# Optimization experiments

Measured on AMD Instinct MI355X. Metric: run time of the kernel, lower is better.

## Reference

```python
import jax, jax.numpy as jnp
import numpy as np

# Module constants (match init_kwargs / input_specs)
B, Q, K, DM, H, F, S = 2, 2048, 2048, 512, 8, 5, 2
DH = DM // H  # head dim = 64


def setup_inputs() -> dict:
    key = jax.random.key(0)
    ks_ = jax.random.split(key, 18)
    sc = 1.0 / np.sqrt(DM)
    inp = {
        'qs': jax.random.normal(ks_[0], (B, Q, DM), jnp.float32),
        'ks': jax.random.normal(ks_[1], (B, K, DM), jnp.float32),
        'vs': jax.random.normal(ks_[2], (B, K, DM), jnp.float32),
        'qs_locs': jax.random.uniform(ks_[3], (B, Q, S), jnp.float32) * 10.0,
        'ks_locs': jax.random.uniform(ks_[4], (B, K, S), jnp.float32) * 10.0,
        # projection weights (MLP([512]) == single Dense(512))
        'Wq': jax.random.normal(ks_[5], (DM, DM), jnp.float32) * sc,
        'bq': jnp.zeros((DM,), jnp.float32),
        'Wk': jax.random.normal(ks_[6], (DM, DM), jnp.float32) * sc,
        'bk': jnp.zeros((DM,), jnp.float32),
        'Wv': jax.random.normal(ks_[7], (DM, DM), jnp.float32) * sc,
        'bv': jnp.zeros((DM,), jnp.float32),
        'Wo': jax.random.normal(ks_[8], (DM, DM), jnp.float32) * sc,
        'bo': jnp.zeros((DM,), jnp.float32),
        # TISA RBF params, one triple per (head, basis); init near module defaults (1,1,0)
        'a': 1.0 + 0.1 * jax.random.normal(ks_[9], (H * F,), jnp.float32),
        'b': 1.0 + 0.1 * jax.random.normal(ks_[10], (H * F,), jnp.float32),
        'c': 0.1 * jax.random.normal(ks_[11], (H * F,), jnp.float32),
        # valid lens in [K//2, K] so every row has at least one valid key
        'valid_lens': jax.random.randint(ks_[12], (B,), K // 2, K + 1).astype(jnp.int32),
    }
    return inp


def reference(qs, ks, vs, qs_locs, ks_locs, Wq, bq, Wk, bk, Wv, bv, Wo, bo, a, b, c, valid_lens):
    # Projections and head split
    q = (qs @ Wq + bq).reshape(B, Q, H, DH) / jnp.sqrt(jnp.float32(DH))
    k = (ks @ Wk + bk).reshape(B, K, H, DH)
    v = (vs @ Wv + bv).reshape(B, K, H, DH)

    # Pairwise L2 distance between query and key locations: [B, Q, K]
    diff = qs_locs[:, :, None, :] - ks_locs[:, None, :, :]
    d = jnp.sqrt(jnp.sum(diff * diff, axis=-1))

    # TISA RBF bias, summed over F basis functions per head: [B, H, Q, K]
    aH, bH, cH = a.reshape(H, F), b.reshape(H, F), c.reshape(H, F)
    bias = jnp.zeros((B, H, Q, K), jnp.float32)
    for f in range(F):  # small fixed loop over basis functions
        af = aH[:, f][None, :, None, None]
        bf = jnp.abs(bH[:, f])[None, :, None, None]
        cf = cH[:, f][None, :, None, None]
        bias = bias + af * jnp.exp(-bf * (d[:, None] - cf) ** 2)

    scores = jnp.einsum('bqhd,bkhd->bhqk', q, k) + bias
    mask = (jnp.arange(K)[None, :] < valid_lens[:, None])[:, None, None, :]  # [B,1,1,K]
    scores = jnp.where(mask, scores, -jnp.inf)
    p = jax.nn.softmax(scores, axis=-1)  # identical to the online-softmax scan result
    ctx = jnp.einsum('bhqk,bkhd->bqhd', p, v).reshape(B, Q, DM)
    return ctx @ Wo + bo
```

## Files before the change

### kernel.cpp

```cpp
#include <hip/hip_runtime.h>
#include <hip/hip_fp16.h>

typedef unsigned short u16;
typedef __bf16 bf16x8 __attribute__((ext_vector_type(8)));
typedef float f32x4 __attribute__((ext_vector_type(4)));
typedef float f32x16 __attribute__((ext_vector_type(16)));

#define MFMA16(a, b, c) __builtin_amdgcn_mfma_f32_16x16x32_bf16(a, b, c, 0, 0, 0)
#define MFMA32(a, b, c) __builtin_amdgcn_mfma_f32_32x32x16_bf16(a, b, c, 0, 0, 0)

constexpr float LOG2E = 1.44269504088896340736f;

__device__ __forceinline__ u16 f2bf(float x) {
  unsigned u = __float_as_uint(x);
  u += 0x7fffu + ((u >> 16) & 1u);
  return (u16)(u >> 16);
}
__device__ __forceinline__ u16 f2bf_fast(float x) {
  return (u16)((__float_as_uint(x) + 0x8000u) >> 16);
}

struct FalseT { static constexpr bool value = false; };
struct TrueT  { static constexpr bool value = true;  };

__global__ void transpose_w_kernel(const float* __restrict__ w0, const float* __restrict__ w1,
                                   const float* __restrict__ w2, const float* __restrict__ w3,
                                   u16* __restrict__ wt) {
  __shared__ float tile[32][33];
  const float* W = blockIdx.z == 0 ? w0 : blockIdx.z == 1 ? w1 : blockIdx.z == 2 ? w2 : w3;
  u16* T = wt + (size_t)blockIdx.z * 512 * 512;
  int tx = threadIdx.x, ty = threadIdx.y;
  int x = blockIdx.x * 32 + tx;
  int y0 = blockIdx.y * 32;
#pragma unroll
  for (int i = 0; i < 32; i += 8) tile[ty + i][tx] = W[(y0 + ty + i) * 512 + x];
  __syncthreads();
  int xo = blockIdx.y * 32 + tx;
  int r0 = blockIdx.x * 32;
#pragma unroll
  for (int i = 0; i < 32; i += 8) T[(r0 + ty + i) * 512 + xo] = f2bf(tile[tx][ty + i]);
}

__global__ __launch_bounds__(256) void qkv_gemm(
    const float* __restrict__ qs, const float* __restrict__ ks, const float* __restrict__ vs,
    const u16* __restrict__ Wt, const float* __restrict__ bq, const float* __restrict__ bk,
    const float* __restrict__ bv, u16* __restrict__ qg, u16* __restrict__ kg,
    u16* __restrict__ vTg) {
  __shared__ u16 As[128 * 72];
  __shared__ u16 Bs[64 * 72];
  const int tid = threadIdx.x;
  const int wave = tid >> 6, lane = tid & 63;
  const int l15 = lane & 15, quad = lane >> 4;
  const int id = blockIdx.x;
  const bool qk = id < 512;
  int z = 0, m0, n0;
  const float* Af = nullptr;
  const u16* Ab = nullptr;
  const u16* Bb = nullptr;
  const float* Bf = nullptr;
  if (qk) {
    z = id >> 8;
    int t = id & 255;
    m0 = (t >> 3) * 128;
    n0 = (t & 7) * 64;
    Af = z ? ks : qs;
    Bb = Wt + z * 262144;
  } else {
    int t = id - 512;
    m0 = (t >> 6) * 128;
    n0 = (t & 63) * 64;
    Ab = Wt + 2 * 262144;
    Bf = vs;
  }
  f32x4 acc[2][4];
#pragma unroll
  for (int i = 0; i < 2; i++)
#pragma unroll
    for (int j = 0; j < 4; j++) {
      f32x4 zr = {0.f, 0.f, 0.f, 0.f};
      acc[i][j] = zr;
    }
  const int srA = tid >> 1, scA = (tid & 1) * 32;
  const int srB = tid >> 2, scB = (tid & 3) * 16;
  for (int k0 = 0; k0 < 512; k0 += 64) {
    if (qk) {
      const float* ga = Af + (m0 + srA) * 512 + k0 + scA;
      u16* la = As + srA * 72 + scA;
#pragma unroll
      for (int c = 0; c < 4; ++c) {
        float4 f0 = *(const float4*)(ga + c * 8);
        float4 f1 = *(const float4*)(ga + c * 8 + 4);
        uint4 u;
        u.x = f2bf(f0.x) | ((unsigned)f2bf(f0.y) << 16);
        u.y = f2bf(f0.z) | ((unsigned)f2bf(f0.w) << 16);
        u.z = f2bf(f1.x) | ((unsigned)f2bf(f1.y) << 16);
        u.w = f2bf(f1.z) | ((unsigned)f2bf(f1.w) << 16);
        *(uint4*)(la + c * 8) = u;
      }
      const u16* gb = Bb + (n0 + srB) * 512 + k0 + scB;
      u16* lb = Bs + srB * 72 + scB;
      *(uint4*)(lb) = *(const uint4*)(gb);
      *(uint4*)(lb + 8) = *(const uint4*)(gb + 8);
    } else {
      const u16* ga = Ab + (m0 + srA) * 512 + k0 + scA;
      u16* la = As + srA * 72 + scA;
#pragma unroll
      for (int c = 0; c < 4; ++c) *(uint4*)(la + c * 8) = *(const uint4*)(ga + c * 8);
      const float* gb = Bf + (n0 + srB) * 512 + k0 + scB;
      u16* lb = Bs + srB * 72 + scB;
#pragma unroll
      for (int c = 0; c < 2; ++c) {
        float4 f0 = *(const float4*)(gb + c * 8);
        float4 f1 = *(const float4*)(gb + c * 8 + 4);
        uint4 u;
        u.x = f2bf(f0.x) | ((unsigned)f2bf(f0.y) << 16);
        u.y = f2bf(f0.z) | ((unsigned)f2bf(f0.w) << 16);
        u.z = f2bf(f1.x) | ((unsigned)f2bf(f1.y) << 16);
        u.w = f2bf(f1.z) | ((unsigned)f2bf(f1.w) << 16);
        *(uint4*)(lb + c * 8) = u;
      }
    }
    __syncthreads();
#pragma unroll
    for (int st = 0; st < 2; ++st) {
      bf16x8 af[2], bfr[4];
#pragma unroll
      for (int mt = 0; mt < 2; ++mt)
        af[mt] = *(const bf16x8*)(As + (wave * 32 + mt * 16 + l15) * 72 + st * 32 + quad * 8);
#pragma unroll
      for (int nt = 0; nt < 4; ++nt)
        bfr[nt] = *(const bf16x8*)(Bs + (nt * 16 + l15) * 72 + st * 32 + quad * 8);
#pragma unroll
      for (int mt = 0; mt < 2; ++mt)
#pragma unroll
        for (int nt = 0; nt < 4; ++nt) acc[mt][nt] = MFMA16(af[mt], bfr[nt], acc[mt][nt]);
    }
    __syncthreads();
  }
  if (qk) {
    const float* bias = z ? bk : bq;
    const float scale = z ? 1.0f : 0.125f * LOG2E;
    u16* outp = z ? kg : qg;
#pragma unroll
    for (int mt = 0; mt < 2; ++mt)
#pragma unroll
      for (int nt = 0; nt < 4; ++nt)
#pragma unroll
        for (int r = 0; r < 4; ++r) {
          int row = m0 + wave * 32 + mt * 16 + quad * 4 + r;
          int col = n0 + nt * 16 + l15;
          float v = (acc[mt][nt][r] + bias[col]) * scale;
          int b = row >> 11, q = row & 2047, h = col >> 6, dh = col & 63;
          outp[(((b * 8 + h) * 2048) + q) * 64 + dh] = f2bf(v);
        }
  } else {
#pragma unroll
    for (int mt = 0; mt < 2; ++mt)
#pragma unroll
      for (int nt = 0; nt < 4; ++nt)
#pragma unroll
        for (int r = 0; r < 4; ++r) {
          int row = m0 + wave * 32 + mt * 16 + quad * 4 + r;
          int col = n0 + nt * 16 + l15;
          vTg[row * 4096 + col] = f2bf(acc[mt][nt][r] + bv[row]);
        }
  }
}

__global__ __launch_bounds__(256, 4) void attn_kernel(
    const u16* __restrict__ qg, const u16* __restrict__ kg, const u16* __restrict__ vTg,
    const float* __restrict__ qlocs, const float* __restrict__ klocs,
    const float* __restrict__ aP, const float* __restrict__ bP, const float* __restrict__ cP,
    const int* __restrict__ vlen, u16* __restrict__ Opart, float* __restrict__ lpart) {
  constexpr int TBLN = 1024;
  constexpr float DMAX = 14.16f;
  constexpr float TSCALE = (float)TBLN / DMAX;
  __shared__ u16 Ks[64 * 72];
  __shared__ u16 Vs[64 * 72];
  __shared__ u16 Ps[4][32 * 68];
  __shared__ alignas(16) float2 kloc_s[64];
  __shared__ unsigned tbl[TBLN];
  const int tid = threadIdx.x;
  const int wave = tid >> 6, lane = tid & 63;
  const int l31 = lane & 31, hi = lane >> 5;
  const int bh = blockIdx.y, b = bh >> 3, h = bh & 7;
  const int z = blockIdx.z;
  const int vl = vlen[b];
  const int ntiles = (vl + 63) >> 6;
  const int nfull = vl >> 6;
  const int tb = ntiles >> 2, rem = ntiles & 3;
  const int kt0 = z * tb + (z < rem ? z : rem);
  const int ktend = kt0 + tb + (z < rem ? 1 : 0);

  for (int i = tid; i < TBLN; i += 256) {
    float d0 = i * (DMAX / TBLN), d1 = (i + 1) * (DMAX / TBLN);
    float g0 = 0.f, g1 = 0.f;
#pragma unroll
    for (int f = 0; f < 5; ++f) {
      float af = aP[h * 5 + f], bf = fabsf(bP[h * 5 + f]), cf = cP[h * 5 + f];
      float t0 = d0 - cf, t1 = d1 - cf;
      g0 += af * __expf(-bf * t0 * t0);
      g1 += af * __expf(-bf * t1 * t1);
    }
    g0 *= LOG2E;
    g1 *= LOG2E;
    unsigned lo = __half_as_ushort(__float2half(g0));
    unsigned hi_ = __half_as_ushort(__float2half(g1 - g0));
    tbl[i] = lo | (hi_ << 16);
  }

  const int qrow = blockIdx.x * 128 + wave * 32 + l31;
  bf16x8 aq[4];
  {
    const u16* qr = qg + (bh * 2048 + qrow) * 64 + hi * 8;
#pragma unroll
    for (int st = 0; st < 4; ++st) aq[st] = *(const bf16x8*)(qr + st * 16);
  }
  float qpx, qpy;
  {
    float2 p = *(const float2*)(qlocs + (b * 2048 + qrow) * 2);
    qpx = p.x * TSCALE;
    qpy = p.y * TSCALE;
  }
  float l_ = 0.f;
  f32x16 oacc[2];
#pragma unroll
  for (int i = 0; i < 2; ++i)
#pragma unroll
    for (int j = 0; j < 16; ++j) oacc[i][j] = 0.f;

  const int srow = tid >> 2, scol = (tid & 3) * 16;
  const u16* gk_base = kg + (bh * 2048 + srow) * 64 + scol;
  const u16* gv_base = vTg + (h * 64 + srow) * 4096 + b * 2048 + scol;
  const float* kl_base = klocs + (b * 2048 + tid) * 2;
  u16* pw = Ps[wave];

  auto tile = [&](int kt, auto mc) {
    constexpr bool MASKED = decltype(mc)::value;
    const int k0 = kt * 64;
    {
      const u16* gk = gk_base + k0 * 64;
      u16* lk = Ks + srow * 72 + scol;
      *(uint4*)(lk) = *(const uint4*)(gk);
      *(uint4*)(lk + 8) = *(const uint4*)(gk + 8);
      const u16* gv = gv_base + k0;
      u16* lv = Vs + srow * 72 + scol;
      *(uint4*)(lv) = *(const uint4*)(gv);
      *(uint4*)(lv + 8) = *(const uint4*)(gv + 8);
      if (tid < 64) {
        float2 kl = *(const float2*)(kl_base + k0 * 2);
        kloc_s[tid] = make_float2(kl.x * TSCALE, kl.y * TSCALE);
      }
    }
    __syncthreads();
    f32x16 s[2];
#pragma unroll
    for (int t = 0; t < 2; ++t) {
#pragma unroll
      for (int j = 0; j < 16; ++j) s[t][j] = 0.f;
#pragma unroll
      for (int st = 0; st < 4; ++st) {
        bf16x8 kf = *(const bf16x8*)(Ks + (t * 32 + l31) * 72 + st * 16 + hi * 8);
        s[t] = MFMA32(kf, aq[st], s[t]);
      }
    }
#pragma unroll
    for (int t = 0; t < 2; ++t)
#pragma unroll
      for (int g = 0; g < 4; ++g) {
        const int kl0 = t * 32 + hi * 4 + g * 8;
        float4 ka = *(const float4*)(&kloc_s[kl0]);
        float4 kb = *(const float4*)(&kloc_s[kl0 + 2]);
        float kx[4] = {ka.x, ka.z, kb.x, kb.z};
        float ky[4] = {ka.y, ka.w, kb.y, kb.w};
        float p[4];
#pragma unroll
        for (int j = 0; j < 4; ++j) {
          float dx = qpx - kx[j], dy = qpy - ky[j];
          float t_ = __builtin_amdgcn_sqrtf(fmaf(dx, dx, dy * dy));
          int ti = (int)t_;
          float fr = t_ - (float)ti;
          unsigned e = tbl[ti];
          float gg = __half2float(__ushort_as_half((u16)(e & 0xffffu)));
          float dg = __half2float(__ushort_as_half((u16)(e >> 16)));
          float v = s[t][g * 4 + j] + fmaf(fr, dg, gg);
          if (MASKED) v = (k0 + kl0 + j < vl) ? v : -1e30f;
          p[j] = __builtin_amdgcn_exp2f(v);
          l_ += p[j];
        }
        uint2 w;
        w.x = f2bf_fast(p[0]) | ((unsigned)f2bf_fast(p[1]) << 16);
        w.y = f2bf_fast(p[2]) | ((unsigned)f2bf_fast(p[3]) << 16);
        *(uint2*)(pw + l31 * 68 + kl0) = w;
      }
    __asm__ volatile("s_waitcnt lgkmcnt(0)" ::: "memory");
#pragma unroll
    for (int st = 0; st < 4; ++st) {
      bf16x8 pf = *(const bf16x8*)(pw + l31 * 68 + st * 16 + hi * 8);
#pragma unroll
      for (int h2 = 0; h2 < 2; ++h2) {
        bf16x8 vf = *(const bf16x8*)(Vs + (h2 * 32 + l31) * 72 + st * 16 + hi * 8);
        oacc[h2] = MFMA32(vf, pf, oacc[h2]);
      }
    }
    __syncthreads();
  };

  const int fullend = ktend < nfull ? ktend : nfull;
  for (int kt = kt0; kt < fullend; ++kt) tile(kt, FalseT{});
  if (ktend > nfull) tile(nfull, TrueT{});

  l_ += __shfl_xor(l_, 32);
  if (hi == 0) lpart[z * 32768 + bh * 2048 + qrow] = l_;
  u16* ob = Opart + ((size_t)(z * 16 + bh) * 2048 + qrow) * 64;
#pragma unroll
  for (int h2 = 0; h2 < 2; ++h2)
#pragma unroll
    for (int g = 0; g < 4; ++g) {
      const int dh0 = h2 * 32 + hi * 4 + g * 8;
      uint2 w;
      w.x = f2bf(oacc[h2][g * 4 + 0]) | ((unsigned)f2bf(oacc[h2][g * 4 + 1]) << 16);
      w.y = f2bf(oacc[h2][g * 4 + 2]) | ((unsigned)f2bf(oacc[h2][g * 4 + 3]) << 16);
      *(uint2*)(ob + dh0) = w;
    }
}

__global__ __launch_bounds__(256) void out_gemm(
    const u16* __restrict__ Opart, const float* __restrict__ lpart,
    const u16* __restrict__ Wt, const float* __restrict__ bo, float* __restrict__ out) {
  __shared__ u16 As[128 * 72];
  __shared__ u16 Bs[64 * 72];
  const u16* WoT = Wt + 3 * 262144;
  const int tid = threadIdx.x;
  const int wave = tid >> 6, lane = tid & 63;
  const int l15 = lane & 15, quad = lane >> 4;
  const int m0 = blockIdx.x * 128, n0 = blockIdx.y * 64;
  f32x4 acc[2][4];
#pragma unroll
  for (int i = 0; i < 2; i++)
#pragma unroll
    for (int j = 0; j < 4; j++) {
      f32x4 zr = {0.f, 0.f, 0.f, 0.f};
      acc[i][j] = zr;
    }
  const int srA = tid >> 1, scA = (tid & 1) * 32;
  const int srB = tid >> 2, scB = (tid & 3) * 16;
  const int row = m0 + srA, b = row >> 11, qq = row & 2047;
  for (int k0 = 0; k0 < 512; k0 += 64) {
    const int h = k0 >> 6;
    const int base = (b * 8 + h) * 2048 + qq;
    float l = lpart[base] + lpart[32768 + base] + lpart[2 * 32768 + base] +
              lpart[3 * 32768 + base];
    const float inv = 1.f / l;
    float vals[32];
#pragma unroll
    for (int e = 0; e < 32; ++e) vals[e] = 0.f;
#pragma unroll
    for (int zz = 0; zz < 4; ++zz) {
      const u16* op = Opart + ((size_t)(zz * 32768) + base) * 64 + scA;
#pragma unroll
      for (int c = 0; c < 4; ++c) {
        bf16x8 o8 = *(const bf16x8*)(op + c * 8);
#pragma unroll
        for (int j = 0; j < 8; ++j) vals[c * 8 + j] += (float)o8[j];
      }
    }
    u16* la = As + srA * 72 + scA;
#pragma unroll
    for (int c = 0; c < 4; ++c) {
      uint4 u;
      u.x = f2bf(vals[c * 8 + 0] * inv) | ((unsigned)f2bf(vals[c * 8 + 1] * inv) << 16);
      u.y = f2bf(vals[c * 8 + 2] * inv) | ((unsigned)f2bf(vals[c * 8 + 3] * inv) << 16);
      u.z = f2bf(vals[c * 8 + 4] * inv) | ((unsigned)f2bf(vals[c * 8 + 5] * inv) << 16);
      u.w = f2bf(vals[c * 8 + 6] * inv) | ((unsigned)f2bf(vals[c * 8 + 7] * inv) << 16);
      *(uint4*)(la + c * 8) = u;
    }
    const u16* gb = WoT + (n0 + srB) * 512 + k0 + scB;
    u16* lb = Bs + srB * 72 + scB;
    *(uint4*)(lb) = *(const uint4*)(gb);
    *(uint4*)(lb + 8) = *(const uint4*)(gb + 8);
    __syncthreads();
#pragma unroll
    for (int st = 0; st < 2; ++st) {
      bf16x8 af[2], bfr[4];
#pragma unroll
      for (int mt = 0; mt < 2; ++mt)
        af[mt] = *(const bf16x8*)(As + (wave * 32 + mt * 16 + l15) * 72 + st * 32 + quad * 8);
#pragma unroll
      for (int nt = 0; nt < 4; ++nt)
        bfr[nt] = *(const bf16x8*)(Bs + (nt * 16 + l15) * 72 + st * 32 + quad * 8);
#pragma unroll
      for (int mt = 0; mt < 2; ++mt)
#pragma unroll
        for (int nt = 0; nt < 4; ++nt) acc[mt][nt] = MFMA16(af[mt], bfr[nt], acc[mt][nt]);
    }
    __syncthreads();
  }
#pragma unroll
  for (int mt = 0; mt < 2; ++mt)
#pragma unroll
    for (int nt = 0; nt < 4; ++nt)
#pragma unroll
      for (int r = 0; r < 4; ++r) {
        int rrow = m0 + wave * 32 + mt * 16 + quad * 4 + r;
        int col = n0 + nt * 16 + l15;
        out[rrow * 512 + col] = acc[mt][nt][r] + bo[col];
      }
}

extern "C" void kernel_launch(void* const* d_in, const int* in_sizes, int n_in, void* d_out,
                              int out_size, void* d_ws, size_t ws_size, hipStream_t stream) {
  const float* qs = (const float*)d_in[0];
  const float* ks = (const float*)d_in[1];
  const float* vs = (const float*)d_in[2];
  const float* qlocs = (const float*)d_in[3];
  const float* klocs = (const float*)d_in[4];
  const float* Wq = (const float*)d_in[5];
  const float* bq = (const float*)d_in[6];
  const float* Wk = (const float*)d_in[7];
  const float* bk = (const float*)d_in[8];
  const float* Wv = (const float*)d_in[9];
  const float* bv = (const float*)d_in[10];
  const float* Wo = (const float*)d_in[11];
  const float* bo = (const float*)d_in[12];
  const float* aP = (const float*)d_in[13];
  const float* bP = (const float*)d_in[14];
  const float* cP = (const float*)d_in[15];
  const int* vlen = (const int*)d_in[16];
  float* out = (float*)d_out;

  u16* Wt = (u16*)d_ws;
  u16* qg = Wt + 4 * 262144;
  u16* kg = qg + 2097152;
  u16* vTg = kg + 2097152;
  u16* Opart = vTg + 2097152;
  float* lpart = (float*)(Opart + (size_t)4 * 2097152);

  transpose_w_kernel<<<dim3(16, 16, 4), dim3(32, 8), 0, stream>>>(Wq, Wk, Wv, Wo, Wt);
  qkv_gemm<<<768, 256, 0, stream>>>(qs, ks, vs, Wt, bq, bk, bv, qg, kg, vTg);
  attn_kernel<<<dim3(16, 16, 4), 256, 0, stream>>>(qg, kg, vTg, qlocs, klocs, aP, bP, cP, vlen,
                                                   Opart, lpart);
  out_gemm<<<dim3(32, 8), 256, 0, stream>>>(Opart, lpart, Wt, bo, out);
}
```

Before: 198.0 us.

## Pre-swizzle K/V into MFMA fragment layout and load directly from global

The projection kernel now writes K and V in a per-tile fragment-ordered layout matching the MFMA operand register layout. The attention kernel then loads K/V fragments straight from global memory into registers, dropping the shared-memory staging of K and V and the two block-wide barriers per tile. Key locations for the block's whole key range are preloaded once into a larger shared buffer. In exchange, every wave in the block re-reads the same K/V from global/L2 (4x redundant traffic), and load latency is no longer hidden behind LDS staging.

```diff
diff --git a/kernel.cpp b/kernel.cpp
--- a/kernel.cpp
+++ b/kernel.cpp
@@ -140,7 +140,6 @@
   if (qk) {
     const float* bias = z ? bk : bq;
     const float scale = z ? 1.0f : 0.125f * LOG2E;
-    u16* outp = z ? kg : qg;
 #pragma unroll
     for (int mt = 0; mt < 2; ++mt)
 #pragma unroll
@@ -150,8 +149,16 @@
           int row = m0 + wave * 32 + mt * 16 + quad * 4 + r;
           int col = n0 + nt * 16 + l15;
           float v = (acc[mt][nt][r] + bias[col]) * scale;
-          int b = row >> 11, q = row & 2047, h = col >> 6, dh = col & 63;
-          outp[(((b * 8 + h) * 2048) + q) * 64 + dh] = f2bf(v);
+          int b = row >> 11, key = row & 2047, hh = col >> 6, dh = col & 63;
+          int bhh = b * 8 + hh;
+          if (z == 0) {
+            qg[((bhh * 2048) + key) * 64 + dh] = f2bf(v);
+          } else {
+            int kt = key >> 6, tt = (key >> 5) & 1, lk = key & 31;
+            int st = dh >> 4, hif = (dh >> 3) & 1, j = dh & 7;
+            kg[(size_t)(bhh * 32 + kt) * 4096 + tt * 2048 + st * 512 + (hif * 32 + lk) * 8 +
+               j] = f2bf(v);
+          }
         }
   } else {
 #pragma unroll
@@ -162,23 +169,26 @@
         for (int r = 0; r < 4; ++r) {
           int row = m0 + wave * 32 + mt * 16 + quad * 4 + r;
           int col = n0 + nt * 16 + l15;
-          vTg[row * 4096 + col] = f2bf(acc[mt][nt][r] + bv[row]);
+          int hh = row >> 6, dh = row & 63, b = col >> 11, key = col & 2047;
+          int bhh = b * 8 + hh;
+          int kt = key >> 6, kk = key & 63, st = kk >> 4, hif = (kk >> 3) & 1, j = kk & 7;
+          int h2 = dh >> 5, lk = dh & 31;
+          vTg[(size_t)(bhh * 32 + kt) * 4096 + h2 * 2048 + st * 512 + (hif * 32 + lk) * 8 + j] =
+              f2bf(acc[mt][nt][r] + bv[row]);
         }
   }
 }
 
 __global__ __launch_bounds__(256, 4) void attn_kernel(
-    const u16* __restrict__ qg, const u16* __restrict__ kg, const u16* __restrict__ vTg,
+    const u16* __restrict__ qg, const u16* __restrict__ kfrag, const u16* __restrict__ vfrag,
     const float* __restrict__ qlocs, const float* __restrict__ klocs,
     const float* __restrict__ aP, const float* __restrict__ bP, const float* __restrict__ cP,
     const int* __restrict__ vlen, u16* __restrict__ Opart, float* __restrict__ lpart) {
   constexpr int TBLN = 1024;
   constexpr float DMAX = 14.16f;
   constexpr float TSCALE = (float)TBLN / DMAX;
-  __shared__ u16 Ks[64 * 72];
-  __shared__ u16 Vs[64 * 72];
   __shared__ u16 Ps[4][32 * 68];
-  __shared__ alignas(16) float2 kloc_s[64];
+  __shared__ alignas(16) float2 klb[640];
   __shared__ unsigned tbl[TBLN];
   const int tid = threadIdx.x;
   const int wave = tid >> 6, lane = tid & 63;
@@ -208,6 +218,12 @@
     unsigned hi_ = __half_as_ushort(__float2half(g1 - g0));
     tbl[i] = lo | (hi_ << 16);
   }
+  const int nk = (ktend - kt0) * 64;
+  for (int i = tid; i < nk; i += 256) {
+    float2 kl = *(const float2*)(klocs + (b * 2048 + kt0 * 64 + i) * 2);
+    klb[i] = make_float2(kl.x * TSCALE, kl.y * TSCALE);
+  }
+  __syncthreads();
 
   const int qrow = blockIdx.x * 128 + wave * 32 + l31;
   bf16x8 aq[4];
@@ -228,49 +244,30 @@
   for (int i = 0; i < 2; ++i)
 #pragma unroll
     for (int j = 0; j < 16; ++j) oacc[i][j] = 0.f;
-
-  const int srow = tid >> 2, scol = (tid & 3) * 16;
-  const u16* gk_base = kg + (bh * 2048 + srow) * 64 + scol;
-  const u16* gv_base = vTg + (h * 64 + srow) * 4096 + b * 2048 + scol;
-  const float* kl_base = klocs + (b * 2048 + tid) * 2;
   u16* pw = Ps[wave];
 
   auto tile = [&](int kt, auto mc) {
     constexpr bool MASKED = decltype(mc)::value;
     const int k0 = kt * 64;
-    {
-      const u16* gk = gk_base + k0 * 64;
-      u16* lk = Ks + srow * 72 + scol;
-      *(uint4*)(lk) = *(const uint4*)(gk);
-      *(uint4*)(lk + 8) = *(const uint4*)(gk + 8);
-      const u16* gv = gv_base + k0;
-      u16* lv = Vs + srow * 72 + scol;
-      *(uint4*)(lv) = *(const uint4*)(gv);
-      *(uint4*)(lv + 8) = *(const uint4*)(gv + 8);
-      if (tid < 64) {
-        float2 kl = *(const float2*)(kl_base + k0 * 2);
-        kloc_s[tid] = make_float2(kl.x * TSCALE, kl.y * TSCALE);
-      }
-    }
-    __syncthreads();
-    f32x16 s[2];
+    const int rt64 = (kt - kt0) * 64;
+    const u16* fb = kfrag + (size_t)(bh * 32 + kt) * 4096 + lane * 8;
+    const u16* vb = vfrag + (size_t)(bh * 32 + kt) * 4096 + lane * 8;
 #pragma unroll
     for (int t = 0; t < 2; ++t) {
-#pragma unroll
-      for (int j = 0; j < 16; ++j) s[t][j] = 0.f;
-#pragma unroll
-      for (int st = 0; st < 4; ++st) {
-        bf16x8 kf = *(const bf16x8*)(Ks + (t * 32 + l31) * 72 + st * 16 + hi * 8);
-        s[t] = MFMA32(kf, aq[st], s[t]);
-      }
-    }
-#pragma unroll
-    for (int t = 0; t < 2; ++t)
+      bf16x8 kf[4];
+#pragma unroll
+      for (int st = 0; st < 4; ++st)
+        kf[st] = *(const bf16x8*)(fb + t * 2048 + st * 512);
+      f32x16 s;
+#pragma unroll
+      for (int j = 0; j < 16; ++j) s[j] = 0.f;
+#pragma unroll
+      for (int st = 0; st < 4; ++st) s = MFMA32(kf[st], aq[st], s);
 #pragma unroll
       for (int g = 0; g < 4; ++g) {
         const int kl0 = t * 32 + hi * 4 + g * 8;
-        float4 ka = *(const float4*)(&kloc_s[kl0]);
-        float4 kb = *(const float4*)(&kloc_s[kl0 + 2]);
+        float4 ka = *(const float4*)(&klb[rt64 + kl0]);
+        float4 kb = *(const float4*)(&klb[rt64 + kl0 + 2]);
         float kx[4] = {ka.x, ka.z, kb.x, kb.z};
         float ky[4] = {ka.y, ka.w, kb.y, kb.w};
         float p[4];
@@ -283,7 +280,7 @@
           unsigned e = tbl[ti];
           float gg = __half2float(__ushort_as_half((u16)(e & 0xffffu)));
           float dg = __half2float(__ushort_as_half((u16)(e >> 16)));
-          float v = s[t][g * 4 + j] + fmaf(fr, dg, gg);
+          float v = s[g * 4 + j] + fmaf(fr, dg, gg);
           if (MASKED) v = (k0 + kl0 + j < vl) ? v : -1e30f;
           p[j] = __builtin_amdgcn_exp2f(v);
           l_ += p[j];
@@ -293,17 +290,20 @@
         w.y = f2bf_fast(p[2]) | ((unsigned)f2bf_fast(p[3]) << 16);
         *(uint2*)(pw + l31 * 68 + kl0) = w;
       }
+    }
     __asm__ volatile("s_waitcnt lgkmcnt(0)" ::: "memory");
+    bf16x8 vf[2][4];
+#pragma unroll
+    for (int h2 = 0; h2 < 2; ++h2)
+#pragma unroll
+      for (int st = 0; st < 4; ++st)
+        vf[h2][st] = *(const bf16x8*)(vb + h2 * 2048 + st * 512);
 #pragma unroll
     for (int st = 0; st < 4; ++st) {
       bf16x8 pf = *(const bf16x8*)(pw + l31 * 68 + st * 16 + hi * 8);
 #pragma unroll
-      for (int h2 = 0; h2 < 2; ++h2) {
-        bf16x8 vf = *(const bf16x8*)(Vs + (h2 * 32 + l31) * 72 + st * 16 + hi * 8);
-        oacc[h2] = MFMA32(vf, pf, oacc[h2]);
-      }
-    }
-    __syncthreads();
+      for (int h2 = 0; h2 < 2; ++h2) oacc[h2] = MFMA32(vf[h2][st], pf, oacc[h2]);
+    }
   };
 
   const int fullend = ktend < nfull ? ktend : nfull;
```

Measured after the change: 203.1 us. 2.6% more time.
